# Kernel tuning notes

Measured on AMD Instinct MI355X. Metric: run time of the kernel, lower is better.

## Reference

```python
import jax, jax.numpy as jnp
import numpy as np

B, T, N = 16, 16, 1024          # patients, max visits, code_num
C, G, H, A, P = 48, 32, 150, 32, 32  # code_size, graph_size, hidden_size, t_attention_size, pool attn size
OUT = 1
NEG = -1e30


def setup_inputs() -> dict:
    key = jax.random.key(0)
    ks = jax.random.split(key, 20)
    code_x = (jax.random.uniform(ks[0], (B, T, N)) < 0.2).astype(jnp.float32)
    neighbors = (jax.random.uniform(ks[1], (B, T, N)) < 0.2).astype(jnp.float32)
    cat = jax.random.randint(ks[2], (B, T, N), 0, 8)
    # divided[..., 0/1/2] = disjoint m1 (persistent) / m2 (emerging-neighbor) / m3 (emerging-unrelated) masks
    divided = jnp.stack([(cat == 0), (cat == 1), (cat == 2)], axis=-1).astype(jnp.int32)
    lens = jax.random.randint(ks[3], (B,), 1, T + 1)
    prior = jax.random.uniform(ks[4], (N,))
    adj = (jax.random.uniform(ks[5], (N, N)) * (jax.random.uniform(ks[6], (N, N)) < 0.05)).astype(jnp.float32)

    def nrm(k, shape, scale=0.05):
        return (jax.random.normal(k, shape) * scale).astype(jnp.float32)

    return dict(
        code_x=code_x, divided=divided, neighbors=neighbors, lens=lens, prior=prior, adj=adj,
        c_emb=nrm(ks[7], (N, C)), n_emb=nrm(ks[8], (N, C)), u_emb=nrm(ks[9], (N, G)),
        Wg=nrm(ks[10], (C, G)), bg=jnp.zeros((G,), jnp.float32),
        W_ih=nrm(ks[11], (3 * H, G)), b_ih=jnp.zeros((3 * H,), jnp.float32),
        W_hh=nrm(ks[12], (3 * H, H)), b_hh=jnp.zeros((3 * H,), jnp.float32),
        Wq=nrm(ks[13], (G, A)), bq=jnp.zeros((A,), jnp.float32),
        Wk=nrm(ks[14], (G, A)), bk=jnp.zeros((A,), jnp.float32),
        Wv=nrm(ks[15], (G, H)), bv=jnp.zeros((H,), jnp.float32),
        Wp=nrm(ks[16], (H, P)), bp=jnp.zeros((P,), jnp.float32),
        ctx=nrm(ks[17], (P,)),
        Wc=nrm(ks[18], (H, OUT)), bc=jnp.zeros((OUT,), jnp.float32),
    )


def _forward(code_x, divided, neighbors, lens, prior, adj, c_emb, n_emb, u_emb,
             Wg, bg, W_ih, b_ih, W_hh, b_hh, Wq, bq, Wk, bk, Wv, bv,
             Wp, bp, ctx, Wc, bc):
    pr = prior[:, None]                                  # [N,1] disease prior scaling of graph messages
    scale = 1.0 / jnp.sqrt(jnp.asarray(A, jnp.float32))

    def gru(x, h):
        # torch nn.GRUCell semantics; x: [B,N,G], h: [B,N,H]
        gi = jnp.einsum('bng,kg->bnk', x, W_ih) + b_ih
        gh = jnp.einsum('bnh,kh->bnk', h, W_hh) + b_hh
        ir, iz, i_n = jnp.split(gi, 3, -1)
        hr, hz, h_n = jnp.split(gh, 3, -1)
        r = jax.nn.sigmoid(ir + hr)
        z = jax.nn.sigmoid(iz + hz)
        cand = jnp.tanh(i_n + r * h_n)
        return (1.0 - z) * cand + z * h

    def step(carry, xs):
        h_prev, no_prev, t = carry
        cx, nb, dv = xs                                  # [B,N], [B,N], [B,N,3]
        c = cx[..., None]
        n = nb[..., None]
        # --- GraphLayer: adjacency message passing, prior-weighted ---
        ce = c * c_emb                                   # [B,N,C]
        ne = n * n_emb
        agg_c = jnp.einsum('mn,bnc->bmc', adj, ce) * pr
        agg_n = jnp.einsum('mn,bnc->bmc', adj, ne) * pr
        co = jax.nn.leaky_relu((ce + c * (agg_c + agg_n)) @ Wg + bg)   # [B,N,G]
        no = jax.nn.leaky_relu((ne + n * (agg_n + agg_c)) @ Wg + bg)
        # --- TransitionLayer ---
        m1 = dv[..., 0] > 0
        m2 = dv[..., 1] > 0
        m3 = dv[..., 2] > 0
        m23 = m2 | m3
        h_gru = gru(co, h_prev)                          # GRU branch for persistent codes (m1)
        # attention branch: queries = prev-step neighbor embeddings (m2) or unrelated embeddings (m3)
        qf = jnp.where(m2[..., None], no_prev, 0.0) + jnp.where(m3[..., None], u_emb, 0.0)
        q = qf @ Wq + bq
        k = co @ Wk + bk
        v = co @ Wv + bv                                 # [B,N,H]
        g = jnp.einsum('bma,bna->bmn', q, k) * scale     # scores over active m2|m3 keys only
        g = jnp.where(m23[:, None, :], g, NEG)
        h_att = jnp.tanh(jnp.einsum('bmn,bnh->bmh', jax.nn.softmax(g, axis=-1), v))
        t_pos = (t > 0).astype(co.dtype)                 # m23 branch only runs for t > 0 (as in original)
        h_new = jnp.where(m1[..., None], h_gru, 0.0) + t_pos * jnp.where(m23[..., None], h_att, 0.0)
        # masked maxes (0 when the index set is empty, as in original)
        om1 = jnp.max(jnp.where(m1[..., None], h_gru, NEG), axis=1)
        om1 = jnp.where(jnp.any(m1, axis=1)[:, None], om1, 0.0)
        om23 = jnp.max(jnp.where(m23[..., None], h_att, NEG), axis=1)
        om23 = jnp.where(jnp.any(m23, axis=1)[:, None], om23, 0.0)
        out_t = om1 + t_pos * om23                       # [B,H]
        return (h_new, no, t + 1), out_t

    h0 = jnp.zeros((B, N, H), jnp.float32)
    no0 = jnp.zeros((B, N, G), jnp.float32)
    xs = (jnp.transpose(code_x, (1, 0, 2)),
          jnp.transpose(neighbors, (1, 0, 2)),
          jnp.transpose(divided, (1, 0, 2, 3)))
    _, outs = jax.lax.scan(step, (h0, no0, jnp.int32(0)), xs)
    outs = jnp.transpose(outs, (1, 0, 2))                # [B,T,H]
    # --- DotProductAttention pooling over valid (ragged) timesteps ---
    vu = (outs @ Wp + bp) @ ctx                          # [B,T]
    valid = jnp.arange(T)[None, :] < lens[:, None]
    score = jax.nn.softmax(jnp.where(valid, vu, NEG), axis=-1)
    pooled = jnp.sum(outs * score[..., None], axis=1)    # [B,H]
    # --- Classifier (dropout identity at eval, activation=None) ---
    return pooled @ Wc + bc


def reference(code_x, divided, neighbors, lens, prior, adj, c_emb, n_emb, u_emb,
              Wg, bg, W_ih, b_ih, W_hh, b_hh, Wq, bq, Wk, bk, Wv, bv,
              Wp, bp, ctx, Wc, bc):
    return _forward(code_x, divided, neighbors, lens, prior, adj, c_emb, n_emb, u_emb,
                    Wg, bg, W_ih, b_ih, W_hh, b_hh, Wq, bq, Wk, bk, Wv, bv,
                    Wp, bp, ctx, Wc, bc)
```

## Files before the change

### kernel.cpp

```cpp
#include <hip/hip_runtime.h>

#define B_ 16
#define T_ 16
#define N_ 1024
#define C_ 48
#define G_ 32
#define H_ 150
#define A_ 32
#define P_ 32
#define H3_ 450
#define NNZ_CAP 262144
#define CAP1 256
#define CAP23 384
#define CHCAP 40960
#define CHCAPL 16384
#define SCALE_ 0.17677669529663687f

__device__ __forceinline__ unsigned fenc(float f){
  unsigned u = __float_as_uint(f);
  return (u & 0x80000000u) ? ~u : (u | 0x80000000u);
}
__device__ __forceinline__ float fdec(unsigned e){
  unsigned u = (e & 0x80000000u) ? (e & 0x7fffffffu) : ~e;
  return __uint_as_float(u);
}
__device__ __forceinline__ float sigmf(float x){ return 1.f/(1.f+__expf(-x)); }
__device__ __forceinline__ float wmaxf(float v){
  #pragma unroll
  for (int d=32; d>0; d>>=1) v = fmaxf(v, __shfl_xor(v,d));
  return v;
}

#define FMA16(W, PTR, ACC) do { \
    const float4* _c4 = (const float4*)(PTR); \
    float4 _c0=_c4[0], _c1=_c4[1], _c2=_c4[2], _c3=_c4[3]; \
    ACC[0]=fmaf((W),_c0.x,ACC[0]); ACC[1]=fmaf((W),_c0.y,ACC[1]); \
    ACC[2]=fmaf((W),_c0.z,ACC[2]); ACC[3]=fmaf((W),_c0.w,ACC[3]); \
    ACC[4]=fmaf((W),_c1.x,ACC[4]); ACC[5]=fmaf((W),_c1.y,ACC[5]); \
    ACC[6]=fmaf((W),_c1.z,ACC[6]); ACC[7]=fmaf((W),_c1.w,ACC[7]); \
    ACC[8]=fmaf((W),_c2.x,ACC[8]); ACC[9]=fmaf((W),_c2.y,ACC[9]); \
    ACC[10]=fmaf((W),_c2.z,ACC[10]); ACC[11]=fmaf((W),_c2.w,ACC[11]); \
    ACC[12]=fmaf((W),_c3.x,ACC[12]); ACC[13]=fmaf((W),_c3.y,ACC[13]); \
    ACC[14]=fmaf((W),_c3.z,ACC[14]); ACC[15]=fmaf((W),_c3.w,ACC[15]); \
  } while(0)

__global__ void k_csr_cnt(const float* __restrict__ adj, int* __restrict__ rcnt){
  int m = blockIdx.x; int tid = threadIdx.x;
  int c = 0;
  for (int n = tid; n < N_; n += 256) c += (adj[(size_t)m*N_+n] != 0.f) ? 1 : 0;
  __shared__ int sr[256];
  sr[tid]=c; __syncthreads();
  for (int s=128; s>0; s>>=1){ if (tid<s) sr[tid]+=sr[tid+s]; __syncthreads(); }
  if (tid==0) rcnt[m]=sr[0];
}
__global__ void k_csr_scan(const int* __restrict__ rcnt, int* __restrict__ rowptr){
  int lane = threadIdx.x;
  int s = 0;
  for (int r=0;r<16;++r) s += rcnt[lane*16+r];
  int incl = s;
  for (int d=1; d<64; d<<=1){ int y = __shfl_up(incl, d); if (lane>=d) incl += y; }
  int run = incl - s;
  for (int r=0;r<16;++r){ rowptr[lane*16+r] = run; run += rcnt[lane*16+r]; }
  if (lane==63) rowptr[N_] = incl;
}
__global__ void k_csr_fill(const float* __restrict__ adj, const float* __restrict__ prior,
                           const int* __restrict__ rowptr,
                           int* __restrict__ ccol, float* __restrict__ cval){
  int m = blockIdx.x; int lane = threadIdx.x;
  int base = rowptr[m];
  float pm = prior[m];
  for (int it=0; it<N_/64; ++it){
    int n = it*64+lane;
    float a = adj[(size_t)m*N_+n];
    bool pnz = (a != 0.f);
    unsigned long long mk = __ballot(pnz);
    if (pnz){
      int idx = base + __popcll(mk & ((1ULL<<lane)-1ULL));
      if (idx < NNZ_CAP){ ccol[idx]=n; cval[idx]=a*pm; }
    }
    base += __popcll(mk);
  }
}

__global__ void k_masks(const int* __restrict__ divided, int* __restrict__ lst23,
                        int* __restrict__ pos1,
                        int* __restrict__ cnt23, int* __restrict__ cnt1){
  int bt = blockIdx.x; int lane = threadIdx.x;
  int base23=0, base1=0;
  for (int it=0; it<N_/64; ++it){
    int n = it*64+lane;
    const int* dv = &divided[((size_t)bt*N_+n)*3];
    int d0=dv[0], d1=dv[1], d2=dv[2];
    bool p23 = (d1>0)||(d2>0); bool p1 = d0>0;
    unsigned long long mk23 = __ballot(p23);
    unsigned long long mk1  = __ballot(p1);
    unsigned long long ltm = (1ULL<<lane)-1ULL;
    if (p23){ int idx = base23 + __popcll(mk23 & ltm); lst23[(size_t)bt*N_+idx]=n; }
    if (p1){ int idx = base1 + __popcll(mk1 & ltm); pos1[(size_t)bt*N_+n]=idx; }
    base23 += __popcll(mk23); base1 += __popcll(mk1);
  }
  if (lane==0){ cnt23[bt]=base23; cnt1[bt]=base1; }
}

__global__ void k_chains(const int* __restrict__ divided,
                         unsigned* __restrict__ chN, int* __restrict__ nchN,
                         unsigned* __restrict__ chH, int* __restrict__ nchH,
                         unsigned* __restrict__ chL, int* __restrict__ nchL){
  int idx = blockIdx.x*256 + threadIdx.x;
  if (idx >= B_*N_) return;
  int b = idx >> 10, n = idx & (N_-1);
  unsigned m1m = 0;
  for (int t=0;t<T_;++t){
    int d0 = divided[(((size_t)(b*T_+t))*N_ + n)*3];
    if (d0>0) m1m |= (1u<<t);
  }
  unsigned heads = m1m & ~(m1m<<1);
  while (heads){
    int t0 = __builtin_ctz(heads); heads &= (heads-1u);
    unsigned run = m1m >> t0;
    int len = __builtin_ctz(~run);
    unsigned enc = ((unsigned)b<<18)|((unsigned)n<<8)|((unsigned)t0<<4)|(unsigned)(len-1);
    int f = 0;
    if (t0 >= 2){
      size_t pidx = ((size_t)(b*T_+t0-1)*N_ + n)*3;
      if ((divided[pidx+1] | divided[pidx+2]) > 0) f = 1;
    }
    if (f){ int i2 = atomicAdd(nchH,1); if (i2 < CHCAP) chH[i2]=enc; }
    else  { int i2 = atomicAdd(nchN,1); if (i2 < CHCAP) chN[i2]=enc; }
    if (len >= 2){
      int i2 = atomicAdd(nchL, 1);
      if (i2 < CHCAPL) chL[i2] = enc;
    }
  }
}

__global__ void k_wt(const float* __restrict__ W_ih, const float* __restrict__ W_hh,
                     const float* __restrict__ Wq, const float* __restrict__ bq,
                     const float* __restrict__ Wk, const float* __restrict__ Wv,
                     float* __restrict__ WihT, float* __restrict__ WhhT,
                     float* __restrict__ Md, float* __restrict__ WvT){
  int idx = blockIdx.x*256+threadIdx.x;
  if (idx < G_*H3_){ int g=idx/H3_, k=idx-g*H3_; WihT[g*H3_+k]=W_ih[(size_t)k*G_+g]; }
  int idx2 = idx - G_*H3_;
  if (idx2>=0 && idx2 < H_*H3_){ int h=idx2/H3_, k=idx2-h*H3_; WhhT[h*H3_+k]=W_hh[(size_t)k*H_+h]; }
  int e = idx - (G_*H3_ + H_*H3_);
  if (e>=0 && e<1024){
    int g=e>>5, gp=e&31;
    float acc=0.f;
    #pragma unroll
    for (int a=0;a<A_;++a) acc = fmaf(Wq[g*A_+a], Wk[gp*A_+a], acc);
    Md[e]=acc;
  }
  int e2 = e - 1024;
  if (e2>=0 && e2<32){
    float acc=0.f;
    #pragma unroll
    for (int a=0;a<A_;++a) acc = fmaf(Wk[e2*A_+a], bq[a], acc);
    Md[1024+e2]=acc;
  }
  int e3 = e - 1056;
  if (e3>=0 && e3 < H_*G_){
    int h = e3>>5, g = e3&31;
    WvT[e3] = Wv[(size_t)g*H_+h];
  }
}

__global__ void k_init(float* __restrict__ om23f, int* __restrict__ nchN,
                       int* __restrict__ nchH, int* __restrict__ nchL){
  int i = blockIdx.x*256+threadIdx.x;
  if (i<B_*T_*H_){ om23f[i]=0.f; }
  if (i==0){ *nchN = 0; *nchH = 0; *nchL = 0; }
}

__global__ __launch_bounds__(256) void k_cono(
    const float* __restrict__ code_x, const float* __restrict__ neighbors,
    const int* __restrict__ divided,
    const int* __restrict__ rowptr, const int* __restrict__ ccol, const float* __restrict__ cval,
    const float* __restrict__ c_emb, const float* __restrict__ n_emb,
    const float* __restrict__ Wg, const float* __restrict__ bg,
    float* __restrict__ co, float* __restrict__ no_)
{
  __shared__ float sCo[4][C_], sNo[4][C_];
  int w = threadIdx.x >> 6, lane = threadIdx.x & 63;
  int gw = blockIdx.x*4 + w;
  int bt = gw >> 10, m = gw & (N_-1);
  int t = bt & (T_-1);
  const int* dv = &divided[(size_t)gw*3];
  int d0=dv[0], d1=dv[1], d2=dv[2];
  bool needCo = (d0|d1|d2) > 0;
  bool needNo = (t < T_-1) && (divided[((size_t)(gw+N_))*3+1] > 0);
  if (!needCo && !needNo) return;
  float cxm = code_x[gw], nbm = neighbors[gw];
  float acc = 0.f;
  bool needAcc = (needCo && cxm!=0.f) || (needNo && nbm!=0.f);
  if (needAcc){
    int s = rowptr[m], e = rowptr[m+1];
    if (s > NNZ_CAP) s = NNZ_CAP;
    if (e > NNZ_CAP) e = NNZ_CAP;
    int btN = bt << 10;
    for (int base = s; base < e; base += 64){
      int j = base + lane;
      int cc = 0; float wx = 0.f, wy = 0.f;
      if (j < e){
        cc = ccol[j];
        float cv = cval[j];
        float xs = code_x[btN+cc], ys = neighbors[btN+cc];
        wx = cv*xs; wy = cv*ys;
      }
      unsigned long long mk = __ballot(wx!=0.f || wy!=0.f);
      while (mk){
        int u0 = __builtin_ctzll(mk); mk &= (mk-1ULL);
        int u1 = -1;
        if (mk){ u1 = __builtin_ctzll(mk); mk &= (mk-1ULL); }
        int u1s = (u1>=0)? u1 : u0;
        int n0 = __shfl(cc,u0); float a0x=__shfl(wx,u0), a0y=__shfl(wy,u0);
        int n1 = __shfl(cc,u1s); float a1x=__shfl(wx,u1s), a1y=__shfl(wy,u1s);
        float ce0=0.f,ne0=0.f,ce1=0.f,ne1=0.f;
        if (lane < C_){
          ce0 = c_emb[(size_t)n0*C_+lane]; ne0 = n_emb[(size_t)n0*C_+lane];
          ce1 = c_emb[(size_t)n1*C_+lane]; ne1 = n_emb[(size_t)n1*C_+lane];
        }
        acc = fmaf(a0x, ce0, acc); acc = fmaf(a0y, ne0, acc);
        if (u1>=0){ acc = fmaf(a1x, ce1, acc); acc = fmaf(a1y, ne1, acc); }
      }
    }
  }
  if (lane < C_){
    sCo[w][lane] = cxm * (c_emb[(size_t)m*C_+lane] + acc);
    sNo[w][lane] = nbm * (n_emb[(size_t)m*C_+lane] + acc);
  }
  asm volatile("s_waitcnt lgkmcnt(0)" ::: "memory");
  int g = lane & 31; bool isNo = lane >= 32;
  const float* src = isNo ? sNo[w] : sCo[w];
  float a2 = bg[g];
  #pragma unroll
  for (int c=0;c<C_;++c) a2 = fmaf(src[c], Wg[c*G_+g], a2);
  float r = a2 >= 0.f ? a2 : 0.01f*a2;
  if (isNo ? needNo : needCo){
    float* dst = isNo ? no_ : co;
    dst[(size_t)gw*G_ + g] = r;
  }
}

__global__ __launch_bounds__(768) void k_attn(
    const float* __restrict__ co, const float* __restrict__ no_,
    const float* __restrict__ u_emb, const int* __restrict__ divided,
    const int* __restrict__ lst23, const int* __restrict__ cnt23, const int* __restrict__ pos1,
    const float* __restrict__ Md, const float* __restrict__ WvT, const float* __restrict__ bv,
    float* __restrict__ hsel, float* __restrict__ om23f)
{
  int b = blockIdx.x; int t = blockIdx.y + 1; int bt = b*T_ + t;
  int cnt = cnt23[bt]; if (cnt > CAP23) cnt = CAP23;
  if (cnt == 0) return;
  __shared__ int   sLst[CAP23];
  __shared__ __align__(16) float sCo[CAP23][G_];
  __shared__ float sL[CAP23];
  __shared__ unsigned sMax[H_];
  int tid = threadIdx.x;
  int grp = (tid >= 384) ? 1 : 0;
  int r   = tid - 384*grp;
  unsigned sent = fenc(-1e30f);
  for (int i=tid; i<cnt; i+=768) sLst[i] = lst23[(size_t)bt*N_+i];
  for (int i=tid; i<H_; i+=768) sMax[i] = sent;
  __syncthreads();
  for (int i=tid; i<cnt*8; i+=768){
    int rrow = i>>3, seg = i&7;
    float4 v = *(const float4*)&co[((((size_t)bt<<10) + sLst[rrow])<<5) + seg*4];
    *(float4*)&sCo[rrow][seg*4] = v;
  }
  bool act = (r < cnt);
  int n = 0;
  float qpp[G_];
  if (act){
    n = sLst[r];
    int d1 = divided[((size_t)bt*N_+n)*3+1];
    const float* qsrc = (d1>0) ? &no_[((((size_t)(bt-1))<<10)+n)<<5] : &u_emb[(size_t)n*G_];
    float4 qv[8];
    #pragma unroll
    for (int j=0;j<8;++j) qv[j] = ((const float4*)qsrc)[j];
    #pragma unroll
    for (int j=0;j<G_;++j) qpp[j] = Md[1024+j];
    #pragma unroll
    for (int g=0; g<G_; ++g){
      float qfg = (g&3)==0 ? qv[g>>2].x : (g&3)==1 ? qv[g>>2].y : (g&3)==2 ? qv[g>>2].z : qv[g>>2].w;
      const float4* mr = (const float4*)&Md[g*G_];
      #pragma unroll
      for (int j=0;j<8;++j){
        float4 mj = mr[j];
        qpp[4*j+0] = fmaf(qfg, mj.x, qpp[4*j+0]);
        qpp[4*j+1] = fmaf(qfg, mj.y, qpp[4*j+1]);
        qpp[4*j+2] = fmaf(qfg, mj.z, qpp[4*j+2]);
        qpp[4*j+3] = fmaf(qfg, mj.w, qpp[4*j+3]);
      }
    }
  } else {
    #pragma unroll
    for (int j=0;j<G_;++j) qpp[j]=0.f;
  }
  __syncthreads();
  int half = (cnt+1)>>1;
  int c0 = grp ? half : 0;
  int c1 = grp ? cnt  : half;
  float pbar[G_]; float l = 0.f;
  #pragma unroll
  for (int j=0;j<G_;++j) pbar[j]=0.f;
  if (act){
    #pragma unroll 2
    for (int c=c0;c<c1;++c){
      const float4* col = (const float4*)&sCo[c][0];
      float4 xv[8];
      #pragma unroll
      for (int j=0;j<8;++j) xv[j]=col[j];
      float d0=0.f,d1v=0.f,d2v=0.f,d3=0.f;
      #pragma unroll
      for (int j=0;j<8;j+=4){
        d0 = fmaf(qpp[4*j+0], xv[j].x, d0); d1v = fmaf(qpp[4*j+1], xv[j].y, d1v);
        d2v = fmaf(qpp[4*j+2], xv[j].z, d2v); d3 = fmaf(qpp[4*j+3], xv[j].w, d3);
        d0 = fmaf(qpp[4*j+4], xv[j+1].x, d0); d1v = fmaf(qpp[4*j+5], xv[j+1].y, d1v);
        d2v = fmaf(qpp[4*j+6], xv[j+1].z, d2v); d3 = fmaf(qpp[4*j+7], xv[j+1].w, d3);
        d0 = fmaf(qpp[4*j+8], xv[j+2].x, d0); d1v = fmaf(qpp[4*j+9], xv[j+2].y, d1v);
        d2v = fmaf(qpp[4*j+10], xv[j+2].z, d2v); d3 = fmaf(qpp[4*j+11], xv[j+2].w, d3);
        d0 = fmaf(qpp[4*j+12], xv[j+3].x, d0); d1v = fmaf(qpp[4*j+13], xv[j+3].y, d1v);
        d2v = fmaf(qpp[4*j+14], xv[j+3].z, d2v); d3 = fmaf(qpp[4*j+15], xv[j+3].w, d3);
      }
      float dot = (d0+d1v)+(d2v+d3);
      float pv = __expf(dot*SCALE_);
      l += pv;
      #pragma unroll
      for (int j=0;j<8;++j){
        pbar[4*j+0] = fmaf(pv, xv[j].x, pbar[4*j+0]);
        pbar[4*j+1] = fmaf(pv, xv[j].y, pbar[4*j+1]);
        pbar[4*j+2] = fmaf(pv, xv[j].z, pbar[4*j+2]);
        pbar[4*j+3] = fmaf(pv, xv[j].w, pbar[4*j+3]);
      }
    }
  }
  __syncthreads();
  if (act && grp==0){
    #pragma unroll
    for (int j=0;j<G_;++j) sCo[r][j] = pbar[j];
    sL[r] = l;
  }
  __syncthreads();
  if (act && grp==1){
    #pragma unroll
    for (int j=0;j<G_;++j) sCo[r][j] += pbar[j];
    sL[r] += l;
  }
  __syncthreads();
  float pb[G_];
  if (act){
    float inv = 1.f / sL[r];
    const float4* pr = (const float4*)&sCo[r][0];
    #pragma unroll
    for (int j=0;j<8;++j){
      float4 pv4 = pr[j];
      pb[4*j+0]=pv4.x*inv; pb[4*j+1]=pv4.y*inv; pb[4*j+2]=pv4.z*inv; pb[4*j+3]=pv4.w*inv;
    }
  } else {
    #pragma unroll
    for (int j=0;j<G_;++j) pb[j]=0.f;
  }
  bool wsel=false; float* hd=nullptr;
  if (act && t+1 < T_){
    size_t nidx = ((size_t)b*T_+(t+1))*N_ + n;
    if (divided[nidx*3+0] > 0){
      int pos = pos1[nidx];
      if (pos >= 0 && pos < CAP1){ wsel=true; hd=&hsel[(((size_t)b*T_+t)*CAP1 + pos)*H_]; }
    }
  }
  int lane = tid & 63;
  int hA = grp*75, hB = hA + 75;
  for (int h=hA; h<hB; ++h){
    float acc = bv[h];
    const float4* wr = (const float4*)&WvT[h*G_];
    #pragma unroll
    for (int j=0;j<8;++j){
      float4 wj = wr[j];
      acc = fmaf(pb[4*j+0], wj.x, acc);
      acc = fmaf(pb[4*j+1], wj.y, acc);
      acc = fmaf(pb[4*j+2], wj.z, acc);
      acc = fmaf(pb[4*j+3], wj.w, acc);
    }
    float o = act ? tanhf(acc) : -1e30f;
    float om = wmaxf(o);
    if (lane==0) atomicMax(&sMax[h], fenc(om));
    if (wsel) hd[h] = o;
  }
  __syncthreads();
  for (int i=tid; i<H_; i+=768) om23f[(size_t)bt*H_+i] = fdec(sMax[i]);
}

__global__ __launch_bounds__(256) void k_gruheadN(
    const float* __restrict__ co, const int* __restrict__ pos1,
    const unsigned* __restrict__ chN, const int* __restrict__ nchN,
    const float* __restrict__ WihT, const float* __restrict__ b_ih,
    const float* __restrict__ b_hh, float* __restrict__ gout)
{
  __shared__ __align__(16) float sCoT[G_][16];
  __shared__ float sG[16][452];
  __shared__ int sBt[16], sN[16], sPos[16];
  int tid = threadIdx.x;
  int NC = *nchN; if (NC > CHCAP) NC = CHCAP;
  int base = blockIdx.x * 16;
  if (base >= NC) return;
  int num = min(16, NC - base);
  if (tid < 16){
    if (tid < num){
      unsigned cl = chN[base+tid];
      int b = cl>>18, n = (cl>>8)&1023, t0 = (cl>>4)&15;
      int bt = b*T_ + t0;
      sBt[tid]=bt; sN[tid]=n; sPos[tid]=pos1[(size_t)bt*N_+n];
    } else { sBt[tid]=0; sN[tid]=0; sPos[tid]=-1; }
  }
  __syncthreads();
  for (int i=tid; i<G_*16; i+=256){
    int g = i>>4, ii = i&15;
    sCoT[g][ii] = (ii<num) ? co[((size_t)sBt[ii]*N_+sN[ii])*G_+g] : 0.f;
  }
  __syncthreads();
  for (int pass=0; pass<2; ++pass){
    int k = pass*256 + tid;
    if (k < H3_){
      float acc[16];
      #pragma unroll
      for (int u=0;u<16;++u) acc[u]=0.f;
      for (int g=0; g<G_; ++g){
        float wih = WihT[g*H3_ + k];
        FMA16(wih, &sCoT[g][0], acc);
      }
      #pragma unroll
      for (int u=0;u<16;++u) sG[u][k] = acc[u];
    }
  }
  __syncthreads();
  for (int i=tid; i<num*152; i+=256){
    int s = i/152, h = i - s*152;
    if (h < H_){
      int pos = sPos[s];
      if (pos >= 0 && pos < CAP1){
        float r = sigmf(sG[s][h]       + b_ih[h]       + b_hh[h]);
        float z = sigmf(sG[s][h+H_]    + b_ih[h+H_]    + b_hh[h+H_]);
        float cand = tanhf(sG[s][h+2*H_] + b_ih[h+2*H_] + r*b_hh[h+2*H_]);
        gout[((size_t)sBt[s]*CAP1 + pos)*H_ + h] = (1.f-z)*cand;
      }
    }
  }
}

__global__ __launch_bounds__(256) void k_gruheadH(
    const float* __restrict__ co, const float* __restrict__ hsel,
    const int* __restrict__ pos1,
    const unsigned* __restrict__ chH, const int* __restrict__ nchH,
    const float* __restrict__ WihT, const float* __restrict__ b_ih,
    const float* __restrict__ WhhT, const float* __restrict__ b_hh,
    float* __restrict__ gout)
{
  __shared__ __align__(16) float sCoT[G_][16];
  __shared__ __align__(16) float sHT[152][16];
  __shared__ float sG[16][452];
  __shared__ float sGhn[16][152];
  __shared__ int sBt[16], sN[16], sPos[16], sHo[16];
  int tid = threadIdx.x;
  int NC = *nchH; if (NC > CHCAP) NC = CHCAP;
  int base = blockIdx.x * 16;
  if (base >= NC) return;
  int num = min(16, NC - base);
  if (tid < 16){
    if (tid < num){
      unsigned cl = chH[base+tid];
      int b = cl>>18, n = (cl>>8)&1023, t0 = (cl>>4)&15;
      int bt = b*T_ + t0;
      int pos = pos1[(size_t)bt*N_+n];
      sBt[tid]=bt; sN[tid]=n; sPos[tid]=pos;
      sHo[tid] = (b*T_ + (t0-1))*CAP1 + ((pos>=0 && pos<CAP1) ? pos : 0);
    } else { sBt[tid]=0; sN[tid]=0; sPos[tid]=-1; sHo[tid]=0; }
  }
  __syncthreads();
  for (int i=tid; i<G_*16; i+=256){
    int g = i>>4, ii = i&15;
    sCoT[g][ii] = (ii<num) ? co[((size_t)sBt[ii]*N_+sN[ii])*G_+g] : 0.f;
  }
  for (int i=tid; i<152*16; i+=256){
    int q = i>>4, ii = i&15;
    float v = 0.f;
    if (ii < num && q < H_) v = hsel[(size_t)sHo[ii]*H_ + q];
    sHT[q][ii] = v;
  }
  __syncthreads();
  for (int pass=0; pass<2; ++pass){
    int k = pass*256 + tid;
    if (k < H3_){
      float acc[16];
      #pragma unroll
      for (int u=0;u<16;++u) acc[u]=0.f;
      for (int g=0; g<G_; ++g){
        float wih = WihT[g*H3_ + k];
        FMA16(wih, &sCoT[g][0], acc);
      }
      #pragma unroll
      for (int u=0;u<16;++u) sG[u][k] = acc[u];
    }
  }
  for (int pass=0; pass<2; ++pass){
    int k = pass*256 + tid;
    if (k < H3_){
      float acc[16];
      #pragma unroll
      for (int u=0;u<16;++u) acc[u]=0.f;
      for (int q=0; q<H_; ++q){
        float whh = WhhT[q*H3_ + k];
        FMA16(whh, &sHT[q][0], acc);
      }
      if (k < 2*H_){
        #pragma unroll
        for (int u=0;u<16;++u) sG[u][k] += acc[u];
      } else {
        #pragma unroll
        for (int u=0;u<16;++u) sGhn[u][k-2*H_] = acc[u];
      }
    }
  }
  __syncthreads();
  for (int i=tid; i<num*152; i+=256){
    int s = i/152, h = i - s*152;
    if (h < H_){
      int pos = sPos[s];
      if (pos >= 0 && pos < CAP1){
        float hv = sHT[h][s];
        float r = sigmf(sG[s][h]       + b_ih[h]       + b_hh[h]);
        float z = sigmf(sG[s][h+H_]    + b_ih[h+H_]    + b_hh[h+H_]);
        float cand = tanhf(sG[s][h+2*H_] + b_ih[h+2*H_] + r*(sGhn[s][h] + b_hh[h+2*H_]));
        float o = (1.f-z)*cand + z*hv;
        gout[((size_t)sBt[s]*CAP1 + pos)*H_ + h] = o;
      }
    }
  }
}

__global__ __launch_bounds__(256) void k_grutail(
    const float* __restrict__ co, const int* __restrict__ pos1,
    const unsigned* __restrict__ chainsL, const int* __restrict__ nchL,
    const float* __restrict__ WihT, const float* __restrict__ b_ih,
    const float* __restrict__ WhhT, const float* __restrict__ b_hh,
    float* __restrict__ gout)
{
  __shared__ float hst[4][4][H_];
  int w = threadIdx.x >> 6, lane = threadIdx.x & 63;
  int NC = *nchL; if (NC > CHCAPL) NC = CHCAPL;
  int cbase = (blockIdx.x*4 + w)*4;
  if (cbase >= NC) return;

  int cbv[4], cnv[4], t0v[4], lenv[4];
  #pragma unroll
  for (int u=0;u<4;++u){
    int cid = cbase+u; bool ca = cid < NC;
    unsigned cl = chainsL[ca ? cid : (NC-1)];
    cbv[u]=cl>>18; cnv[u]=(cl>>8)&1023; t0v[u]=(cl>>4)&15;
    lenv[u]= ca ? (int)((cl&15)+1) : 1;
  }
  int maxlen = lenv[0];
  #pragma unroll
  for (int u=1;u<4;++u) maxlen = max(maxlen, lenv[u]);

  int h0=lane,h1=lane+64,h2=lane+128; bool has2=(h2<H_); int h2c=has2?h2:0;
  float bi[9], bh[9];
  bi[0]=b_ih[h0]; bi[1]=b_ih[h0+H_]; bi[2]=b_ih[h0+2*H_];
  bi[3]=b_ih[h1]; bi[4]=b_ih[h1+H_]; bi[5]=b_ih[h1+2*H_];
  bi[6]=b_ih[h2c]; bi[7]=b_ih[h2c+H_]; bi[8]=b_ih[h2c+2*H_];
  bh[0]=b_hh[h0]; bh[1]=b_hh[h0+H_]; bh[2]=b_hh[h0+2*H_];
  bh[3]=b_hh[h1]; bh[4]=b_hh[h1+H_]; bh[5]=b_hh[h1+2*H_];
  bh[6]=b_hh[h2c]; bh[7]=b_hh[h2c+H_]; bh[8]=b_hh[h2c+2*H_];

  for (int s=1; s<maxlen; ++s){
    bool as[4]; int btv[4];
    const float* hp[4];
    #pragma unroll
    for (int u=0;u<4;++u){
      as[u] = s < lenv[u];
      int t = t0v[u] + (as[u] ? s : 0);
      btv[u] = cbv[u]*T_ + t;
      if (s == 1 && as[u]){
        int btp = btv[u] - 1;
        int posp = pos1[(size_t)btp*N_ + cnv[u]];
        if (posp < 0 || posp >= CAP1) posp = 0;
        hp[u] = &gout[((size_t)btp*CAP1 + posp)*H_];
      } else {
        hp[u] = &hst[w][u][0];
      }
    }
    float gi[4][9], gh[4][9];
    #pragma unroll
    for (int u=0;u<4;++u){
      #pragma unroll
      for (int j=0;j<9;++j){ gi[u][j]=bi[j]; gh[u][j]=bh[j]; }
    }
    const float* cop[4];
    #pragma unroll
    for (int u=0;u<4;++u) cop[u] = &co[((size_t)btv[u]*N_ + cnv[u])*G_];
    for (int g=0; g<G_; ++g){
      const float* wr = &WihT[g*H3_];
      float wv[9];
      wv[0]=wr[h0]; wv[1]=wr[h0+H_]; wv[2]=wr[h0+2*H_];
      wv[3]=wr[h1]; wv[4]=wr[h1+H_]; wv[5]=wr[h1+2*H_];
      wv[6]=wr[h2c]; wv[7]=wr[h2c+H_]; wv[8]=wr[h2c+2*H_];
      #pragma unroll
      for (int u=0;u<4;++u){
        float cg = cop[u][g];
        #pragma unroll
        for (int j=0;j<9;++j) gi[u][j]=fmaf(cg, wv[j], gi[u][j]);
      }
    }
    for (int q=0;q<H_;++q){
      const float* wr=&WhhT[q*H3_];
      float wv[9];
      wv[0]=wr[h0]; wv[1]=wr[h0+H_]; wv[2]=wr[h0+2*H_];
      wv[3]=wr[h1]; wv[4]=wr[h1+H_]; wv[5]=wr[h1+2*H_];
      wv[6]=wr[h2c]; wv[7]=wr[h2c+H_]; wv[8]=wr[h2c+2*H_];
      #pragma unroll
      for (int u=0;u<4;++u){
        float hv = hp[u][q];
        #pragma unroll
        for (int j=0;j<9;++j) gh[u][j]=fmaf(hv, wv[j], gh[u][j]);
      }
    }
    #pragma unroll
    for (int u=0;u<4;++u){
      if (as[u]){
        float hv0 = hp[u][h0];
        float hv1 = hp[u][h1];
        float hv2 = has2 ? hp[u][h2] : 0.f;
        float r0=sigmf(gi[u][0]+gh[u][0]), z0=sigmf(gi[u][1]+gh[u][1]);
        float cd0=tanhf(gi[u][2]+r0*gh[u][2]);
        float o0=(1.f-z0)*cd0 + z0*hv0;
        float r1=sigmf(gi[u][3]+gh[u][3]), z1=sigmf(gi[u][4]+gh[u][4]);
        float cd1=tanhf(gi[u][5]+r1*gh[u][5]);
        float o1=(1.f-z1)*cd1 + z1*hv1;
        float o2=0.f;
        if (has2){
          float r2=sigmf(gi[u][6]+gh[u][6]), z2=sigmf(gi[u][7]+gh[u][7]);
          float cd2=tanhf(gi[u][8]+r2*gh[u][8]);
          o2=(1.f-z2)*cd2 + z2*hv2;
        }
        float* hd = &hst[w][u][0];
        hd[h0]=o0; hd[h1]=o1; if (has2) hd[h2]=o2;
        int pos = pos1[(size_t)btv[u]*N_ + cnv[u]];
        if (pos >= 0 && pos < CAP1){
          float* gd = &gout[((size_t)btv[u]*CAP1 + pos)*H_];
          gd[h0]=o0; gd[h1]=o1; if (has2) gd[h2]=o2;
        }
      }
    }
    asm volatile("s_waitcnt lgkmcnt(0)" ::: "memory");
  }
}

__global__ __launch_bounds__(256) void k_om1(
    const float* __restrict__ gout, const int* __restrict__ cnt1, float* __restrict__ om1f)
{
  int bt = blockIdx.x; int tid = threadIdx.x;
  int c1 = cnt1[bt]; if (c1 > CAP1) c1 = CAP1;
  if (tid < H_){
    float mx = -1e30f;
    for (int r=0;r<c1;++r) mx = fmaxf(mx, gout[((size_t)bt*CAP1+r)*H_+tid]);
    om1f[(size_t)bt*H_+tid] = (c1>0) ? mx : 0.f;
  }
}

__global__ __launch_bounds__(256) void k_final(
    const float* __restrict__ om1f, const float* __restrict__ om23f,
    const float* __restrict__ Wp, const float* __restrict__ bp,
    const float* __restrict__ ctx, const float* __restrict__ Wc, const float* __restrict__ bc,
    const int* __restrict__ lens, float* __restrict__ out)
{
  int b = blockIdx.x; int tid = threadIdx.x;
  __shared__ float sOut[T_][H_];
  __shared__ float sTP[T_][P_];
  __shared__ float sVu[T_], sSc[T_], sPool[H_];
  __shared__ float sRed[256];
  for (int i=tid; i<T_*H_; i+=256){
    int t=i/H_, h=i-t*H_;
    float o1 = om1f[((size_t)b*T_+t)*H_+h];
    float o2 = (t>0)? om23f[((size_t)b*T_+t)*H_+h] : 0.f;
    sOut[t][h]=o1+o2;
  }
  __syncthreads();
  for (int pr = tid; pr < T_*P_; pr += 256){
    int t = pr / P_, p = pr - t*P_;
    float acc = bp[p];
    for (int h=0;h<H_;++h) acc = fmaf(sOut[t][h], Wp[h*P_+p], acc);
    sTP[t][p] = acc * ctx[p];
  }
  __syncthreads();
  if (tid < T_){
    float v=0.f;
    for (int p=0;p<P_;++p) v += sTP[tid][p];
    sVu[tid]=v;
  }
  __syncthreads();
  if (tid==0){
    int L = lens[b]; if (L<1) L=1; if (L>T_) L=T_;
    float mx=-1e30f;
    for (int t=0;t<L;++t) mx = fmaxf(mx, sVu[t]);
    float s=0.f;
    for (int t=0;t<L;++t){ float e=__expf(sVu[t]-mx); sSc[t]=e; s+=e; }
    float inv=1.f/s;
    for (int t=0;t<T_;++t) sSc[t] = (t<L)? sSc[t]*inv : 0.f;
  }
  __syncthreads();
  if (tid < H_){
    float acc=0.f;
    for (int t=0;t<T_;++t) acc = fmaf(sOut[t][tid], sSc[t], acc);
    sPool[tid]=acc;
  }
  __syncthreads();
  float v = (tid<H_)? sPool[tid]*Wc[tid] : 0.f;
  sRed[tid]=v; __syncthreads();
  for (int s=128;s>0;s>>=1){ if (tid<s) sRed[tid]+=sRed[tid+s]; __syncthreads(); }
  if (tid==0) out[b] = sRed[0] + bc[0];
}

extern "C" void kernel_launch(void* const* d_in, const int* in_sizes, int n_in,
                              void* d_out, int out_size, void* d_ws, size_t ws_size,
                              hipStream_t stream)
{
  const float* code_x=(const float*)d_in[0];
  const int*   divided=(const int*)d_in[1];
  const float* neighbors=(const float*)d_in[2];
  const int*   lens=(const int*)d_in[3];
  const float* prior=(const float*)d_in[4];
  const float* adj=(const float*)d_in[5];
  const float* c_emb=(const float*)d_in[6];
  const float* n_emb=(const float*)d_in[7];
  const float* u_emb=(const float*)d_in[8];
  const float* Wg=(const float*)d_in[9];
  const float* bg=(const float*)d_in[10];
  const float* W_ih=(const float*)d_in[11];
  const float* b_ih=(const float*)d_in[12];
  const float* W_hh=(const float*)d_in[13];
  const float* b_hh=(const float*)d_in[14];
  const float* Wq=(const float*)d_in[15];
  const float* bq=(const float*)d_in[16];
  const float* Wk=(const float*)d_in[17];
  const float* bk=(const float*)d_in[18];
  const float* Wv=(const float*)d_in[19];
  const float* bv=(const float*)d_in[20];
  const float* Wp=(const float*)d_in[21];
  const float* bp=(const float*)d_in[22];
  const float* ctx=(const float*)d_in[23];
  const float* Wc=(const float*)d_in[24];
  const float* bc=(const float*)d_in[25];
  float* out=(float*)d_out;
  (void)in_sizes; (void)n_in; (void)out_size; (void)ws_size; (void)bk;

  char* p=(char*)d_ws;
  size_t off=0;
  auto carve=[&](size_t bytes)->char*{ char* r=p+off; off=(off+bytes+255)&~(size_t)255; return r; };
  int*   rowptr=(int*)carve((N_+1)*4);
  int*   rcnt  =(int*)carve(N_*4);
  int*   ccol  =(int*)carve((size_t)NNZ_CAP*4);
  float* cval  =(float*)carve((size_t)NNZ_CAP*4);
  int*   cnt23 =(int*)carve(B_*T_*4);
  int*   cnt1  =(int*)carve(B_*T_*4);
  int*   lst23 =(int*)carve((size_t)B_*T_*N_*4);
  int*   pos1  =(int*)carve((size_t)B_*T_*N_*4);
  float* co    =(float*)carve((size_t)B_*T_*N_*G_*4);
  float* no_   =(float*)carve((size_t)B_*T_*N_*G_*4);
  float* WihT  =(float*)carve((size_t)G_*H3_*4);
  float* WhhT  =(float*)carve((size_t)H_*H3_*4);
  float* Md    =(float*)carve(1056*4);
  float* WvT   =(float*)carve((size_t)H_*G_*4);
  float* hsel  =(float*)carve((size_t)B_*T_*CAP1*H_*4);
  float* gout  =(float*)carve((size_t)B_*T_*CAP1*H_*4);
  unsigned* chainsN=(unsigned*)carve((size_t)CHCAP*4);
  unsigned* chainsH=(unsigned*)carve((size_t)CHCAP*4);
  unsigned* chainsL=(unsigned*)carve((size_t)CHCAPL*4);
  int*   nchN  =(int*)carve(256);
  int*   nchH  =(int*)carve(256);
  int*   nchL  =(int*)carve(256);
  float* om1f  =(float*)carve((size_t)B_*T_*H_*4);
  float* om23f =(float*)carve((size_t)B_*T_*H_*4);

  k_csr_cnt<<<N_,256,0,stream>>>(adj, rcnt);
  k_csr_scan<<<1,64,0,stream>>>(rcnt, rowptr);
  k_csr_fill<<<N_,64,0,stream>>>(adj, prior, rowptr, ccol, cval);
  k_masks<<<B_*T_,64,0,stream>>>(divided, lst23, pos1, cnt23, cnt1);
  k_wt<<<343,256,0,stream>>>(W_ih, W_hh, Wq, bq, Wk, Wv, WihT, WhhT, Md, WvT);
  k_init<<<(B_*T_*H_+255)/256,256,0,stream>>>(om23f, nchN, nchH, nchL);
  k_chains<<<(B_*N_+255)/256,256,0,stream>>>(divided, chainsN, nchN, chainsH, nchH, chainsL, nchL);
  k_cono<<<B_*T_*N_/4,256,0,stream>>>(code_x, neighbors, divided, rowptr, ccol, cval,
                                      c_emb, n_emb, Wg, bg, co, no_);
  k_attn<<<dim3(B_, T_-1),768,0,stream>>>(co, no_, u_emb, divided,
                                      lst23, cnt23, pos1, Md, WvT, bv,
                                      hsel, om23f);
  k_gruheadN<<<CHCAP/16,256,0,stream>>>(co, pos1, chainsN, nchN,
                                      WihT, b_ih, b_hh, gout);
  k_gruheadH<<<CHCAP/16,256,0,stream>>>(co, hsel, pos1, chainsH, nchH,
                                      WihT, b_ih, WhhT, b_hh, gout);
  k_grutail<<<CHCAPL/16,256,0,stream>>>(co, pos1, chainsL, nchL,
                                      WihT, b_ih, WhhT, b_hh, gout);
  k_om1<<<B_*T_,256,0,stream>>>(gout, cnt1, om1f);
  k_final<<<B_,256,0,stream>>>(om1f, om23f, Wp,bp,ctx,Wc,bc, lens, out);
}
```

Measured before the change: 479.0 us.

## Split GRU chain tails into per-level batched kernels with shared-memory GEMM

Replaces the single tail kernel, where each wavefront walked up to 4 chains serially through every timestep, with 15 per-level launches. Each launch processes all chains at one step offset in batches of 16, staging inputs and hidden states transposed in shared memory so each thread computes one gate column for 16 chains. The aim is more parallelism and better weight reuse than the long serial per-chain loop, at the cost of 15 extra kernel launches and fixed per-level capacity caps that could drop chains. It also rotates the shared-memory index in the attention reduction to reduce bank conflicts.

```diff
diff --git a/kernel.cpp b/kernel.cpp
--- a/kernel.cpp
+++ b/kernel.cpp
@@ -13,7 +13,6 @@
 #define CAP1 256
 #define CAP23 384
 #define CHCAP 40960
-#define CHCAPL 16384
 #define SCALE_ 0.17677669529663687f
 
 __device__ __forceinline__ unsigned fenc(float f){
@@ -30,6 +29,8 @@
   for (int d=32; d>0; d>>=1) v = fmaxf(v, __shfl_xor(v,d));
   return v;
 }
+__device__ __forceinline__ int lvoff(int lv){ return lv==1?0 : (lv==2?8192 : 10240 + (lv-3)*512); }
+__device__ __forceinline__ int lvcap(int lv){ return lv==1?8192 : (lv==2?2048 : 512); }
 
 #define FMA16(W, PTR, ACC) do { \
     const float4* _c4 = (const float4*)(PTR); \
@@ -105,7 +106,7 @@
 __global__ void k_chains(const int* __restrict__ divided,
                          unsigned* __restrict__ chN, int* __restrict__ nchN,
                          unsigned* __restrict__ chH, int* __restrict__ nchH,
-                         unsigned* __restrict__ chL, int* __restrict__ nchL){
+                         unsigned* __restrict__ chLv, int* __restrict__ nLv){
   int idx = blockIdx.x*256 + threadIdx.x;
   if (idx >= B_*N_) return;
   int b = idx >> 10, n = idx & (N_-1);
@@ -127,9 +128,9 @@
     }
     if (f){ int i2 = atomicAdd(nchH,1); if (i2 < CHCAP) chH[i2]=enc; }
     else  { int i2 = atomicAdd(nchN,1); if (i2 < CHCAP) chN[i2]=enc; }
-    if (len >= 2){
-      int i2 = atomicAdd(nchL, 1);
-      if (i2 < CHCAPL) chL[i2] = enc;
+    for (int lv=1; lv<len; ++lv){
+      int i2 = atomicAdd(&nLv[lv], 1);
+      if (i2 < lvcap(lv)) chLv[lvoff(lv) + i2] = enc;
     }
   }
 }
@@ -166,10 +167,11 @@
 }
 
 __global__ void k_init(float* __restrict__ om23f, int* __restrict__ nchN,
-                       int* __restrict__ nchH, int* __restrict__ nchL){
+                       int* __restrict__ nchH, int* __restrict__ nLv){
   int i = blockIdx.x*256+threadIdx.x;
   if (i<B_*T_*H_){ om23f[i]=0.f; }
-  if (i==0){ *nchN = 0; *nchH = 0; *nchL = 0; }
+  if (i==0){ *nchN = 0; *nchH = 0; }
+  if (i<16) nLv[i]=0;
 }
 
 __global__ __launch_bounds__(256) void k_cono(
@@ -338,25 +340,21 @@
   __syncthreads();
   if (act && grp==0){
     #pragma unroll
-    for (int j=0;j<G_;++j) sCo[r][j] = pbar[j];
+    for (int j=0;j<G_;++j) sCo[r][(j+r)&31] = pbar[j];
     sL[r] = l;
   }
   __syncthreads();
   if (act && grp==1){
     #pragma unroll
-    for (int j=0;j<G_;++j) sCo[r][j] += pbar[j];
+    for (int j=0;j<G_;++j) sCo[r][(j+r)&31] += pbar[j];
     sL[r] += l;
   }
   __syncthreads();
   float pb[G_];
   if (act){
     float inv = 1.f / sL[r];
-    const float4* pr = (const float4*)&sCo[r][0];
-    #pragma unroll
-    for (int j=0;j<8;++j){
-      float4 pv4 = pr[j];
-      pb[4*j+0]=pv4.x*inv; pb[4*j+1]=pv4.y*inv; pb[4*j+2]=pv4.z*inv; pb[4*j+3]=pv4.w*inv;
-    }
+    #pragma unroll
+    for (int j=0;j<G_;++j) pb[j] = sCo[r][(j+r)&31] * inv;
   } else {
     #pragma unroll
     for (int j=0;j<G_;++j) pb[j]=0.f;
@@ -538,120 +536,94 @@
   }
 }
 
-__global__ __launch_bounds__(256) void k_grutail(
+__global__ __launch_bounds__(256) void k_grulev(
     const float* __restrict__ co, const int* __restrict__ pos1,
-    const unsigned* __restrict__ chainsL, const int* __restrict__ nchL,
+    const unsigned* __restrict__ chLv, const int* __restrict__ nLv,
     const float* __restrict__ WihT, const float* __restrict__ b_ih,
     const float* __restrict__ WhhT, const float* __restrict__ b_hh,
-    float* __restrict__ gout)
+    float* __restrict__ gout, int s, int cap)
 {
-  __shared__ float hst[4][4][H_];
-  int w = threadIdx.x >> 6, lane = threadIdx.x & 63;
-  int NC = *nchL; if (NC > CHCAPL) NC = CHCAPL;
-  int cbase = (blockIdx.x*4 + w)*4;
-  if (cbase >= NC) return;
-
-  int cbv[4], cnv[4], t0v[4], lenv[4];
-  #pragma unroll
-  for (int u=0;u<4;++u){
-    int cid = cbase+u; bool ca = cid < NC;
-    unsigned cl = chainsL[ca ? cid : (NC-1)];
-    cbv[u]=cl>>18; cnv[u]=(cl>>8)&1023; t0v[u]=(cl>>4)&15;
-    lenv[u]= ca ? (int)((cl&15)+1) : 1;
-  }
-  int maxlen = lenv[0];
-  #pragma unroll
-  for (int u=1;u<4;++u) maxlen = max(maxlen, lenv[u]);
-
-  int h0=lane,h1=lane+64,h2=lane+128; bool has2=(h2<H_); int h2c=has2?h2:0;
-  float bi[9], bh[9];
-  bi[0]=b_ih[h0]; bi[1]=b_ih[h0+H_]; bi[2]=b_ih[h0+2*H_];
-  bi[3]=b_ih[h1]; bi[4]=b_ih[h1+H_]; bi[5]=b_ih[h1+2*H_];
-  bi[6]=b_ih[h2c]; bi[7]=b_ih[h2c+H_]; bi[8]=b_ih[h2c+2*H_];
-  bh[0]=b_hh[h0]; bh[1]=b_hh[h0+H_]; bh[2]=b_hh[h0+2*H_];
-  bh[3]=b_hh[h1]; bh[4]=b_hh[h1+H_]; bh[5]=b_hh[h1+2*H_];
-  bh[6]=b_hh[h2c]; bh[7]=b_hh[h2c+H_]; bh[8]=b_hh[h2c+2*H_];
-
-  for (int s=1; s<maxlen; ++s){
-    bool as[4]; int btv[4];
-    const float* hp[4];
-    #pragma unroll
-    for (int u=0;u<4;++u){
-      as[u] = s < lenv[u];
-      int t = t0v[u] + (as[u] ? s : 0);
-      btv[u] = cbv[u]*T_ + t;
-      if (s == 1 && as[u]){
-        int btp = btv[u] - 1;
-        int posp = pos1[(size_t)btp*N_ + cnv[u]];
-        if (posp < 0 || posp >= CAP1) posp = 0;
-        hp[u] = &gout[((size_t)btp*CAP1 + posp)*H_];
+  __shared__ __align__(16) float sCoT[G_][16];
+  __shared__ __align__(16) float sHT[152][16];
+  __shared__ float sG[16][452];
+  __shared__ float sGhn[16][152];
+  __shared__ int sBt[16], sN[16], sPos[16], sHo[16];
+  int tid = threadIdx.x;
+  int NC = *nLv; if (NC > cap) NC = cap;
+  int base = blockIdx.x * 16;
+  if (base >= NC) return;
+  int num = min(16, NC - base);
+  if (tid < 16){
+    if (tid < num){
+      unsigned cl = chLv[base+tid];
+      int b = cl>>18, n = (cl>>8)&1023, t0 = (cl>>4)&15;
+      int bt = b*T_ + t0 + s;
+      int pos = pos1[(size_t)bt*N_+n];
+      int posp = pos1[(size_t)(bt-1)*N_+n];
+      if (posp < 0 || posp >= CAP1) posp = 0;
+      sBt[tid]=bt; sN[tid]=n; sPos[tid]=pos;
+      sHo[tid] = (bt-1)*CAP1 + posp;
+    } else { sBt[tid]=0; sN[tid]=0; sPos[tid]=-1; sHo[tid]=0; }
+  }
+  __syncthreads();
+  for (int i=tid; i<G_*16; i+=256){
+    int g = i>>4, ii = i&15;
+    sCoT[g][ii] = (ii<num) ? co[((size_t)sBt[ii]*N_+sN[ii])*G_+g] : 0.f;
+  }
+  for (int i=tid; i<152*16; i+=256){
+    int q = i>>4, ii = i&15;
+    float v = 0.f;
+    if (ii < num && q < H_) v = gout[(size_t)sHo[ii]*H_ + q];
+    sHT[q][ii] = v;
+  }
+  __syncthreads();
+  for (int pass=0; pass<2; ++pass){
+    int k = pass*256 + tid;
+    if (k < H3_){
+      float acc[16];
+      #pragma unroll
+      for (int u=0;u<16;++u) acc[u]=0.f;
+      for (int g=0; g<G_; ++g){
+        float wih = WihT[g*H3_ + k];
+        FMA16(wih, &sCoT[g][0], acc);
+      }
+      #pragma unroll
+      for (int u=0;u<16;++u) sG[u][k] = acc[u];
+    }
+  }
+  for (int pass=0; pass<2; ++pass){
+    int k = pass*256 + tid;
+    if (k < H3_){
+      float acc[16];
+      #pragma unroll
+      for (int u=0;u<16;++u) acc[u]=0.f;
+      for (int q=0; q<H_; ++q){
+        float whh = WhhT[q*H3_ + k];
+        FMA16(whh, &sHT[q][0], acc);
+      }
+      if (k < 2*H_){
+        #pragma unroll
+        for (int u=0;u<16;++u) sG[u][k] += acc[u];
       } else {
-        hp[u] = &hst[w][u][0];
-      }
-    }
-    float gi[4][9], gh[4][9];
-    #pragma unroll
-    for (int u=0;u<4;++u){
-      #pragma unroll
-      for (int j=0;j<9;++j){ gi[u][j]=bi[j]; gh[u][j]=bh[j]; }
-    }
-    const float* cop[4];
-    #pragma unroll
-    for (int u=0;u<4;++u) cop[u] = &co[((size_t)btv[u]*N_ + cnv[u])*G_];
-    for (int g=0; g<G_; ++g){
-      const float* wr = &WihT[g*H3_];
-      float wv[9];
-      wv[0]=wr[h0]; wv[1]=wr[h0+H_]; wv[2]=wr[h0+2*H_];
-      wv[3]=wr[h1]; wv[4]=wr[h1+H_]; wv[5]=wr[h1+2*H_];
-      wv[6]=wr[h2c]; wv[7]=wr[h2c+H_]; wv[8]=wr[h2c+2*H_];
-      #pragma unroll
-      for (int u=0;u<4;++u){
-        float cg = cop[u][g];
         #pragma unroll
-        for (int j=0;j<9;++j) gi[u][j]=fmaf(cg, wv[j], gi[u][j]);
-      }
-    }
-    for (int q=0;q<H_;++q){
-      const float* wr=&WhhT[q*H3_];
-      float wv[9];
-      wv[0]=wr[h0]; wv[1]=wr[h0+H_]; wv[2]=wr[h0+2*H_];
-      wv[3]=wr[h1]; wv[4]=wr[h1+H_]; wv[5]=wr[h1+2*H_];
-      wv[6]=wr[h2c]; wv[7]=wr[h2c+H_]; wv[8]=wr[h2c+2*H_];
-      #pragma unroll
-      for (int u=0;u<4;++u){
-        float hv = hp[u][q];
-        #pragma unroll
-        for (int j=0;j<9;++j) gh[u][j]=fmaf(hv, wv[j], gh[u][j]);
-      }
-    }
-    #pragma unroll
-    for (int u=0;u<4;++u){
-      if (as[u]){
-        float hv0 = hp[u][h0];
-        float hv1 = hp[u][h1];
-        float hv2 = has2 ? hp[u][h2] : 0.f;
-        float r0=sigmf(gi[u][0]+gh[u][0]), z0=sigmf(gi[u][1]+gh[u][1]);
-        float cd0=tanhf(gi[u][2]+r0*gh[u][2]);
-        float o0=(1.f-z0)*cd0 + z0*hv0;
-        float r1=sigmf(gi[u][3]+gh[u][3]), z1=sigmf(gi[u][4]+gh[u][4]);
-        float cd1=tanhf(gi[u][5]+r1*gh[u][5]);
-        float o1=(1.f-z1)*cd1 + z1*hv1;
-        float o2=0.f;
-        if (has2){
-          float r2=sigmf(gi[u][6]+gh[u][6]), z2=sigmf(gi[u][7]+gh[u][7]);
-          float cd2=tanhf(gi[u][8]+r2*gh[u][8]);
-          o2=(1.f-z2)*cd2 + z2*hv2;
-        }
-        float* hd = &hst[w][u][0];
-        hd[h0]=o0; hd[h1]=o1; if (has2) hd[h2]=o2;
-        int pos = pos1[(size_t)btv[u]*N_ + cnv[u]];
-        if (pos >= 0 && pos < CAP1){
-          float* gd = &gout[((size_t)btv[u]*CAP1 + pos)*H_];
-          gd[h0]=o0; gd[h1]=o1; if (has2) gd[h2]=o2;
-        }
-      }
-    }
-    asm volatile("s_waitcnt lgkmcnt(0)" ::: "memory");
+        for (int u=0;u<16;++u) sGhn[u][k-2*H_] = acc[u];
+      }
+    }
+  }
+  __syncthreads();
+  for (int i=tid; i<num*152; i+=256){
+    int sl = i/152, h = i - sl*152;
+    if (h < H_){
+      int pos = sPos[sl];
+      if (pos >= 0 && pos < CAP1){
+        float hv = sHT[h][sl];
+        float r = sigmf(sG[sl][h]       + b_ih[h]       + b_hh[h]);
+        float z = sigmf(sG[sl][h+H_]    + b_ih[h+H_]    + b_hh[h+H_]);
+        float cand = tanhf(sG[sl][h+2*H_] + b_ih[h+2*H_] + r*(sGhn[sl][h] + b_hh[h+2*H_]));
+        float o = (1.f-z)*cand + z*hv;
+        gout[((size_t)sBt[sl]*CAP1 + pos)*H_ + h] = o;
+      }
+    }
   }
 }
 
@@ -774,10 +746,10 @@
   float* gout  =(float*)carve((size_t)B_*T_*CAP1*H_*4);
   unsigned* chainsN=(unsigned*)carve((size_t)CHCAP*4);
   unsigned* chainsH=(unsigned*)carve((size_t)CHCAP*4);
-  unsigned* chainsL=(unsigned*)carve((size_t)CHCAPL*4);
+  unsigned* chLv  =(unsigned*)carve((size_t)16896*4);
   int*   nchN  =(int*)carve(256);
   int*   nchH  =(int*)carve(256);
-  int*   nchL  =(int*)carve(256);
+  int*   nLv   =(int*)carve(256);
   float* om1f  =(float*)carve((size_t)B_*T_*H_*4);
   float* om23f =(float*)carve((size_t)B_*T_*H_*4);
 
@@ -786,8 +758,8 @@
   k_csr_fill<<<N_,64,0,stream>>>(adj, prior, rowptr, ccol, cval);
   k_masks<<<B_*T_,64,0,stream>>>(divided, lst23, pos1, cnt23, cnt1);
   k_wt<<<343,256,0,stream>>>(W_ih, W_hh, Wq, bq, Wk, Wv, WihT, WhhT, Md, WvT);
-  k_init<<<(B_*T_*H_+255)/256,256,0,stream>>>(om23f, nchN, nchH, nchL);
-  k_chains<<<(B_*N_+255)/256,256,0,stream>>>(divided, chainsN, nchN, chainsH, nchH, chainsL, nchL);
+  k_init<<<(B_*T_*H_+255)/256,256,0,stream>>>(om23f, nchN, nchH, nLv);
+  k_chains<<<(B_*N_+255)/256,256,0,stream>>>(divided, chainsN, nchN, chainsH, nchH, chLv, nLv);
   k_cono<<<B_*T_*N_/4,256,0,stream>>>(code_x, neighbors, divided, rowptr, ccol, cval,
                                       c_emb, n_emb, Wg, bg, co, no_);
   k_attn<<<dim3(B_, T_-1),768,0,stream>>>(co, no_, u_emb, divided,
@@ -797,8 +769,12 @@
                                       WihT, b_ih, b_hh, gout);
   k_gruheadH<<<CHCAP/16,256,0,stream>>>(co, hsel, pos1, chainsH, nchH,
                                       WihT, b_ih, WhhT, b_hh, gout);
-  k_grutail<<<CHCAPL/16,256,0,stream>>>(co, pos1, chainsL, nchL,
-                                      WihT, b_ih, WhhT, b_hh, gout);
+  for (int s=1; s<=15; ++s){
+    int offv = (s==1)?0:((s==2)?8192:10240+(s-3)*512);
+    int capv = (s==1)?8192:((s==2)?2048:512);
+    k_grulev<<<capv/16,256,0,stream>>>(co, pos1, chLv+offv, nLv+s,
+                                      WihT, b_ih, WhhT, b_hh, gout, s, capv);
+  }
   k_om1<<<B_*T_,256,0,stream>>>(gout, cnt1, om1f);
   k_final<<<B_,256,0,stream>>>(om1f, om23f, Wp,bp,ctx,Wc,bc, lens, out);
 }
```

Result: no change. 481.2 us (+0.5%).
